# Kernel optimization log

Hardware: AMD Instinct MI355X
Metric: run time of the kernel (lower is better)

## Reference

```python
import jax, jax.numpy as jnp
import numpy as np

B, S, E = 8, 4096, 128

def _prelu(x, a):
    return jnp.where(x >= 0, x, a * x)

def setup_inputs() -> dict:
    key = jax.random.key(0)
    ks = jax.random.split(key, 7)
    lim = 1.0 / np.sqrt(E)
    x = jax.random.normal(ks[0], (B, S, E), dtype=jnp.float32)
    Wq = jax.random.uniform(ks[1], (E, E), jnp.float32, -lim, lim)
    Wk = jax.random.uniform(ks[2], (E, E), jnp.float32, -lim, lim)
    Wv = jax.random.uniform(ks[3], (E, E), jnp.float32, -lim, lim)
    bq = jax.random.uniform(ks[4], (E,), jnp.float32, -lim, lim)
    bk = jax.random.uniform(ks[5], (E,), jnp.float32, -lim, lim)
    bv = jax.random.uniform(ks[6], (E,), jnp.float32, -lim, lim)
    # PReLU default: single shared slope initialized to 0.25
    aq = jnp.array(0.25, dtype=jnp.float32)
    ak = jnp.array(0.25, dtype=jnp.float32)
    av = jnp.array(0.25, dtype=jnp.float32)
    return {"x": x, "Wq": Wq, "bq": bq, "aq": aq,
            "Wk": Wk, "bk": bk, "ak": ak,
            "Wv": Wv, "bv": bv, "av": av}

def reference(x, Wq, bq, aq, Wk, bk, ak, Wv, bv, av):
    # Linear (y = x @ W.T + b) followed by PReLU, per nn.Sequential(Linear, PReLU)
    qx = _prelu(jnp.einsum('bse,fe->bsf', x, Wq) + bq, aq)  # [B,S,E]
    kx = _prelu(jnp.einsum('bse,fe->bsf', x, Wk) + bk, ak)
    vx = _prelu(jnp.einsum('bse,fe->bsf', x, Wv) + bv, av)
    scale = 1.0 / jnp.sqrt(jnp.asarray(E, dtype=x.dtype))
    qk = jnp.einsum('bqe,bke->bqk', qx, kx) * scale  # [B,S,S]
    attn = jax.nn.softmax(qk, axis=2)
    return jnp.einsum('bqk,bke->bqe', attn, vx)  # [B,S,E]
```

## Files before the change

kernel.cpp:

```cpp
#include <hip/hip_runtime.h>
#include <hip/hip_bf16.h>
#include <stdint.h>

typedef __bf16 bf16x8 __attribute__((ext_vector_type(8)));
typedef float f32x4 __attribute__((ext_vector_type(4)));
typedef float f32x16 __attribute__((ext_vector_type(16)));
typedef unsigned int u32x4 __attribute__((ext_vector_type(4)));

static constexpr int Bn = 8, Sn = 4096, En = 128;

__device__ __forceinline__ unsigned short f2bf(float f) {
  unsigned u = __builtin_bit_cast(unsigned, f);
  u += 0x7fffu + ((u >> 16) & 1u);
  return (unsigned short)(u >> 16);
}

__device__ __forceinline__ unsigned cvtpk(float a, float b) {
  unsigned r;
  asm("v_cvt_pk_bf16_f32 %0, %1, %2" : "=v"(r) : "v"(a), "v"(b));
  return r;
}

__device__ __forceinline__ void plswap(unsigned &a, unsigned &b) {
  asm("v_permlane32_swap_b32 %0, %1" : "+v"(a), "+v"(b));
}

__global__ __launch_bounds__(256) void qkv_kernel(
    const float* __restrict__ x,
    const float* __restrict__ Wq, const float* __restrict__ bq, const float* __restrict__ aq,
    const float* __restrict__ Wk, const float* __restrict__ bk, const float* __restrict__ ak,
    const float* __restrict__ Wv, const float* __restrict__ bv, const float* __restrict__ av,
    unsigned short* __restrict__ qo, unsigned short* __restrict__ kf,
    unsigned short* __restrict__ vf)
{
  __shared__ __align__(16) unsigned short xs[64 * 136];
  __shared__ __align__(16) unsigned short wsh[128 * 136];
  const int tid = threadIdx.x;
  const int r0 = blockIdx.x * 64;

  for (int i = 0; i < 8; ++i) {
    int cid = tid + i * 256;
    int row = cid >> 5, c4 = cid & 31;
    const float4 v = *(const float4*)&x[(size_t)(r0 + row) * 128 + c4 * 4];
    unsigned short* d = &xs[row * 136 + c4 * 4];
    d[0] = f2bf(v.x); d[1] = f2bf(v.y); d[2] = f2bf(v.z); d[3] = f2bf(v.w);
  }

  const int lane = tid & 63, wid = tid >> 6;
  const int g = lane >> 4, ln = lane & 15;
  const float* Ws[3] = {Wq, Wk, Wv};
  const float* Bs[3] = {bq, bk, bv};
  const float* As[3] = {aq, ak, av};
  bf16x8 afrag[4];

  for (int mat = 0; mat < 3; ++mat) {
    __syncthreads();
    for (int i = 0; i < 16; ++i) {
      int cid = tid + i * 256;
      int row = cid >> 5, c4 = cid & 31;
      const float4 v = *(const float4*)&Ws[mat][row * 128 + c4 * 4];
      unsigned short* d = &wsh[row * 136 + c4 * 4];
      d[0] = f2bf(v.x); d[1] = f2bf(v.y); d[2] = f2bf(v.z); d[3] = f2bf(v.w);
    }
    __syncthreads();

    if (mat == 0) {
      for (int ks = 0; ks < 4; ++ks)
        afrag[ks] = *(const bf16x8*)&xs[(wid * 16 + ln) * 136 + ks * 32 + g * 8];
    }
    const float alpha = As[mat][0];
    f32x4 acc[8];
    for (int nt = 0; nt < 8; ++nt) acc[nt] = (f32x4)(0.f);
    for (int nt = 0; nt < 8; ++nt)
      for (int ks = 0; ks < 4; ++ks) {
        bf16x8 bfrag = *(const bf16x8*)&wsh[(nt * 16 + ln) * 136 + ks * 32 + g * 8];
        acc[nt] = __builtin_amdgcn_mfma_f32_16x16x32_bf16(afrag[ks], bfrag, acc[nt], 0, 0, 0);
      }
    const int mbase = r0 + wid * 16 + g * 4;
    for (int nt = 0; nt < 8; ++nt) {
      const int n = nt * 16 + ln;
      const float bias = Bs[mat][n];
      float vv[4];
      for (int r = 0; r < 4; ++r) {
        float t = acc[nt][r] + bias;
        vv[r] = t >= 0.f ? t : alpha * t;
      }
      if (mat == 0) {
        for (int r = 0; r < 4; ++r) qo[(size_t)(mbase + r) * 128 + n] = f2bf(vv[r]);
      } else if (mat == 1) {
        for (int r = 0; r < 4; ++r) {
          const int key = mbase + r, bb = key >> 12, sl = key & 4095;
          const size_t addr = ((size_t)bb << 20) + (size_t)(sl >> 5) * 8192
                            + nt * 1024 + ((ln >> 3) & 1) * 512
                            + (sl & 31) * 16 + ((ln & 7) << 1);
          *(unsigned short*)((char*)kf + addr) = f2bf(vv[r]);
        }
      } else {
        const int bb = mbase >> 12, sl = mbase & 4095;
        const int kb64 = sl >> 6, kk = sl & 63;
        const int ks2 = kk >> 4, hi2 = (kk >> 3) & 1, j0 = kk & 7;
        const size_t addr = ((size_t)bb << 20) + (size_t)kb64 * 16384
                          + (n >> 5) * 4096 + ks2 * 1024 + hi2 * 512
                          + (n & 31) * 16 + (j0 << 1);
        ushort4 pk;
        pk.x = f2bf(vv[0]); pk.y = f2bf(vv[1]); pk.z = f2bf(vv[2]); pk.w = f2bf(vv[3]);
        *(ushort4*)((char*)vf + addr) = pk;
      }
    }
  }
}

__device__ __forceinline__ void load_frag(const char* kfb, const char* vfb, int kt,
                                          int tid, uint4* kr, uint4* vr) {
  const char* ks = kfb + (size_t)kt * 16384;
  const char* vs = vfb + (size_t)kt * 16384;
  kr[0] = *(const uint4*)(ks + tid * 16);
  kr[1] = *(const uint4*)(ks + 8192 + tid * 16);
  vr[0] = *(const uint4*)(vs + tid * 16);
  vr[1] = *(const uint4*)(vs + 8192 + tid * 16);
}

__device__ __forceinline__ void store_frag(char* slot, int tid,
                                           const uint4* kr, const uint4* vr) {
  *(uint4*)(slot + tid * 16) = kr[0];
  *(uint4*)(slot + 8192 + tid * 16) = kr[1];
  *(uint4*)(slot + 16384 + tid * 16) = vr[0];
  *(uint4*)(slot + 24576 + tid * 16) = vr[1];
}

template <int KSPLIT>
__global__ __launch_bounds__(512, 2) void attn_kernel(
    const unsigned short* __restrict__ q,
    const unsigned short* __restrict__ kf,
    const unsigned short* __restrict__ vf,
    float* __restrict__ opart, float* __restrict__ mpart,
    float* __restrict__ lpart, float* __restrict__ out)
{
  __shared__ __align__(16) char smem[98304];
  const int tid = threadIdx.x;
  const int lane = tid & 63, wid = tid >> 6;
  const int NS = 8 * KSPLIT;
  const int bid = blockIdx.x;
  const int s_ = bid % NS;
  const int qt = bid / NS;
  const int b  = s_ / KSPLIT;
  const int kh = s_ % KSPLIT;
  const int hi = lane >> 5, ln = lane & 31;
  const size_t bOff = (size_t)b * Sn * En;

  const int nkt = (Sn / KSPLIT) / 64;
  const int kbase = kh * (Sn / KSPLIT);
  const char* kfb = (const char*)kf + ((size_t)b << 20) + (size_t)(kbase >> 5) * 8192;
  const char* vfb = (const char*)vf + ((size_t)b << 20) + (size_t)(kbase >> 6) * 16384;

  const int qrow = qt * 256 + wid * 32 + ln;
  bf16x8 qf[8];
  #pragma unroll
  for (int s = 0; s < 8; ++s)
    qf[s] = *(const bf16x8*)((const char*)(q + bOff) + (size_t)qrow * 256 + s * 32 + hi * 16);

  f32x16 acc[4];
  #pragma unroll
  for (int et = 0; et < 4; ++et) acc[et] = (f32x16)(0.f);
  float m_run = -1e30f, lsum = 0.f;

  const float cst = 1.4426950408889634f * 0.08838834764831845f;

  auto qk = [&](const char* slot, f32x16& st0, f32x16& st1) {
    const char* kp = slot + hi * 512 + ln * 16;
    st0 = (f32x16)(0.f); st1 = (f32x16)(0.f);
    __builtin_amdgcn_s_setprio(1);
    #pragma unroll
    for (int s = 0; s < 8; ++s) {
      bf16x8 kf0 = *(const bf16x8*)(kp + s * 1024);
      bf16x8 kf1 = *(const bf16x8*)(kp + 8192 + s * 1024);
      st0 = __builtin_amdgcn_mfma_f32_32x32x16_bf16(kf0, qf[s], st0, 0, 0, 0);
      st1 = __builtin_amdgcn_mfma_f32_32x32x16_bf16(kf1, qf[s], st1, 0, 0, 0);
    }
    __builtin_amdgcn_s_setprio(0);
  };

  auto sm_pv = [&](const char* slot, const f32x16& st0, const f32x16& st1) {
    const char* vp = slot + 16384 + hi * 512 + ln * 16;
    float t16[16];
    #pragma unroll
    for (int i = 0; i < 16; ++i) t16[i] = fmaxf(st0[i], st1[i]);
    float t8[8];
    #pragma unroll
    for (int i = 0; i < 8; ++i) t8[i] = fmaxf(t16[i], t16[i + 8]);
    float t4[4];
    #pragma unroll
    for (int i = 0; i < 4; ++i) t4[i] = fmaxf(t8[i], t8[i + 4]);
    float vtile = fmaxf(fmaxf(t4[0], t4[1]), fmaxf(t4[2], t4[3])) * cst;
    vtile = fmaxf(vtile, __shfl_xor(vtile, 32));

    if (__any(vtile > m_run + 8.0f)) {
      float mnew = fmaxf(m_run, vtile);
      float al = __builtin_amdgcn_exp2f(m_run - mnew);
      #pragma unroll
      for (int et = 0; et < 4; ++et) acc[et] *= al;
      lsum *= al;
      m_run = mnew;
    }

    float p[32];
    #pragma unroll
    for (int i = 0; i < 16; ++i) p[i]      = __builtin_amdgcn_exp2f(fmaf(st0[i], cst, -m_run));
    #pragma unroll
    for (int i = 0; i < 16; ++i) p[16 + i] = __builtin_amdgcn_exp2f(fmaf(st1[i], cst, -m_run));

    float s16[16];
    #pragma unroll
    for (int i = 0; i < 16; ++i) s16[i] = p[i] + p[16 + i];
    float s8[8];
    #pragma unroll
    for (int i = 0; i < 8; ++i) s8[i] = s16[i] + s16[i + 8];
    float s4[4];
    #pragma unroll
    for (int i = 0; i < 4; ++i) s4[i] = s8[i] + s8[i + 4];
    float tsum = (s4[0] + s4[1]) + (s4[2] + s4[3]);
    tsum += __shfl_xor(tsum, 32);
    lsum += tsum;

    unsigned wa[8], wb[8];
    #pragma unroll
    for (int g2 = 0; g2 < 8; ++g2) {
      wa[g2] = cvtpk(p[4 * g2], p[4 * g2 + 1]);
      wb[g2] = cvtpk(p[4 * g2 + 2], p[4 * g2 + 3]);
    }
    bf16x8 pb[4];
    #pragma unroll
    for (int ks = 0; ks < 4; ++ks) {
      unsigned w0 = wa[2 * ks], w2 = wa[2 * ks + 1];
      plswap(w0, w2);
      unsigned w1 = wb[2 * ks], w3 = wb[2 * ks + 1];
      plswap(w1, w3);
      u32x4 w = {w0, w1, w2, w3};
      pb[ks] = __builtin_bit_cast(bf16x8, w);
    }

    __builtin_amdgcn_s_setprio(1);
    #pragma unroll
    for (int ks = 0; ks < 4; ++ks) {
      #pragma unroll
      for (int et = 0; et < 4; ++et) {
        bf16x8 vfr = *(const bf16x8*)(vp + et * 4096 + ks * 1024);
        acc[et] = __builtin_amdgcn_mfma_f32_32x32x16_bf16(vfr, pb[ks], acc[et], 0, 0, 0);
      }
    }
    __builtin_amdgcn_s_setprio(0);
  };

  char* s0 = smem;
  char* s1 = smem + 32768;
  char* s2 = smem + 65536;

  uint4 kregA[2], vregA[2], kregB[2], vregB[2];
  load_frag(kfb, vfb, 0, tid, kregA, vregA);
  store_frag(s0, tid, kregA, vregA);
  load_frag(kfb, vfb, 1, tid, kregB, vregB);
  store_frag(s1, tid, kregB, vregB);
  if (nkt > 2) load_frag(kfb, vfb, 2, tid, kregA, vregA);
  __syncthreads();
  f32x16 sA0, sA1, sB0, sB1;
  qk(s0, sA0, sA1);

  for (int t = 0; t < nkt; t += 2) {
    if (t + 2 < nkt) store_frag(s2, tid, kregA, vregA);
    if (t + 3 < nkt) load_frag(kfb, vfb, t + 3, tid, kregB, vregB);
    qk(s1, sB0, sB1);
    sm_pv(s0, sA0, sA1);
    __syncthreads();

    if (t + 3 < nkt) store_frag(s0, tid, kregB, vregB);
    if (t + 4 < nkt) load_frag(kfb, vfb, t + 4, tid, kregA, vregA);
    if (t + 2 < nkt) qk(s2, sA0, sA1);
    sm_pv(s1, sB0, sB1);
    __syncthreads();

    char* tt = s0; s0 = s2; s2 = s1; s1 = tt;
  }

  if (KSPLIT > 1 && lane < 32) {
    const size_t idx = (size_t)kh * (Bn * Sn) + (size_t)b * Sn + qt * 256 + wid * 32 + ln;
    mpart[idx] = m_run;
    lpart[idx] = lsum;
  }

  __syncthreads();
  const float inv = (KSPLIT == 1) ? (1.0f / lsum) : 1.0f;
  char* sl = smem + wid * 8192;
  char* outb;
  if (KSPLIT == 1)
    outb = (char*)(out + ((size_t)b * Sn + qt * 256 + wid * 32) * En);
  else
    outb = (char*)(opart + ((size_t)kh * (Bn * Sn) + (size_t)b * Sn + qt * 256 + wid * 32) * En);

  #pragma unroll
  for (int h = 0; h < 2; ++h) {
    #pragma unroll
    for (int e2 = 0; e2 < 2; ++e2) {
      const int et = 2 * h + e2;
      #pragma unroll
      for (int rg = 0; rg < 4; ++rg) {
        f32x4 v;
        #pragma unroll
        for (int j = 0; j < 4; ++j) v[j] = acc[et][rg * 4 + j] * inv;
        const int addr = ln * 256 + e2 * 128 + rg * 32 + hi * 16;
        *(f32x4*)(sl + (addr ^ ((ln & 7) << 4))) = v;
      }
    }
    asm volatile("s_waitcnt lgkmcnt(0)" ::: "memory");
    __builtin_amdgcn_sched_barrier(0);
    #pragma unroll
    for (int i = 0; i < 8; ++i) {
      const int flat = i * 1024 + lane * 16;
      const int qr = flat >> 8, col = flat & 255;
      f32x4 v = *(const f32x4*)(sl + ((qr * 256 + col) ^ ((qr & 7) << 4)));
      *(f32x4*)(outb + (size_t)qr * 512 + h * 256 + col) = v;
    }
    if (h == 0) {
      asm volatile("s_waitcnt lgkmcnt(0)" ::: "memory");
      __builtin_amdgcn_sched_barrier(0);
    }
  }
}

template <int NSPLIT>
__global__ __launch_bounds__(256) void combine_kernel(
    const float* __restrict__ op, const float* __restrict__ mp,
    const float* __restrict__ lp, float* __restrict__ out)
{
  const int idx = blockIdx.x * 256 + threadIdx.x;
  const int row = idx >> 5;
  const int BS = Bn * Sn;
  const size_t NO = (size_t)BS * En / 4;
  float m = -1e30f;
  #pragma unroll
  for (int j = 0; j < NSPLIT; ++j) m = fmaxf(m, mp[j * BS + row]);
  float den = 0.f;
  f32x4 sum = (f32x4)(0.f);
  #pragma unroll
  for (int j = 0; j < NSPLIT; ++j) {
    const float w = __builtin_amdgcn_exp2f(mp[j * BS + row] - m);
    den += w * lp[j * BS + row];
    f32x4 o = ((const f32x4*)op)[j * NO + idx];
    sum += o * w;
  }
  const float inv = 1.f / den;
  ((f32x4*)out)[idx] = sum * inv;
}

extern "C" void kernel_launch(void* const* d_in, const int* in_sizes, int n_in,
                              void* d_out, int out_size, void* d_ws, size_t ws_size,
                              hipStream_t stream) {
  const float* x  = (const float*)d_in[0];
  const float* Wq = (const float*)d_in[1];
  const float* bq = (const float*)d_in[2];
  const float* aq = (const float*)d_in[3];
  const float* Wk = (const float*)d_in[4];
  const float* bk = (const float*)d_in[5];
  const float* ak = (const float*)d_in[6];
  const float* Wv = (const float*)d_in[7];
  const float* bv = (const float*)d_in[8];
  const float* av = (const float*)d_in[9];

  const size_t BSE = (size_t)Bn * Sn * En;
  const size_t BS  = (size_t)Bn * Sn;
  char* base = (char*)d_ws;
  unsigned short* qws = (unsigned short*)base;
  unsigned short* kws = qws + BSE;
  unsigned short* vws = kws + BSE;
  const size_t fixed = 3 * BSE * 2;
  float* opart = (float*)(base + fixed);

  auto need = [&](int j) { return fixed + (size_t)j * BSE * 4 + (size_t)j * BS * 8; };
  int split = 1;
  if (ws_size >= need(2)) split = 2;

  float* mpart = (float*)(base + fixed + (size_t)split * BSE * 4);
  float* lpart = mpart + (size_t)split * BS;

  qkv_kernel<<<512, 256, 0, stream>>>(x, Wq, bq, aq, Wk, bk, ak, Wv, bv, av,
                                      qws, kws, vws);
  if (split == 2) {
    attn_kernel<2><<<256, 512, 0, stream>>>(qws, kws, vws, opart, mpart, lpart,
                                            (float*)d_out);
    combine_kernel<2><<<4096, 256, 0, stream>>>(opart, mpart, lpart, (float*)d_out);
  } else {
    attn_kernel<1><<<128, 512, 0, stream>>>(qws, kws, vws, opart, mpart, lpart,
                                            (float*)d_out);
  }
}
```

Before: 142.8 us.

## Load K fragments directly from global into registers, staging only V in LDS

K tiles are no longer staged through shared memory. Each wave now loads its own K fragments straight from global memory into a 16-register prefetch buffer, one tile ahead of the QK MFMAs, and only V goes through the triple-buffered LDS ring. This cuts LDS traffic and shrinks shared memory from 96KB to 64KB. In exchange, every wave reads the same K tile from global/L2 separately (8x redundancy per block) and register pressure rises under the 512x2 launch bounds.

```diff
diff --git a/kernel.cpp b/kernel.cpp
--- a/kernel.cpp
+++ b/kernel.cpp
@@ -110,22 +110,15 @@
   }
 }
 
-__device__ __forceinline__ void load_frag(const char* kfb, const char* vfb, int kt,
-                                          int tid, uint4* kr, uint4* vr) {
-  const char* ks = kfb + (size_t)kt * 16384;
+__device__ __forceinline__ void load_vfrag(const char* vfb, int kt, int tid, uint4* vr) {
   const char* vs = vfb + (size_t)kt * 16384;
-  kr[0] = *(const uint4*)(ks + tid * 16);
-  kr[1] = *(const uint4*)(ks + 8192 + tid * 16);
   vr[0] = *(const uint4*)(vs + tid * 16);
   vr[1] = *(const uint4*)(vs + 8192 + tid * 16);
 }
 
-__device__ __forceinline__ void store_frag(char* slot, int tid,
-                                           const uint4* kr, const uint4* vr) {
-  *(uint4*)(slot + tid * 16) = kr[0];
-  *(uint4*)(slot + 8192 + tid * 16) = kr[1];
-  *(uint4*)(slot + 16384 + tid * 16) = vr[0];
-  *(uint4*)(slot + 24576 + tid * 16) = vr[1];
+__device__ __forceinline__ void store_vfrag(char* slot, int tid, const uint4* vr) {
+  *(uint4*)(slot + tid * 16) = vr[0];
+  *(uint4*)(slot + 8192 + tid * 16) = vr[1];
 }
 
 template <int KSPLIT>
@@ -136,7 +129,7 @@
     float* __restrict__ opart, float* __restrict__ mpart,
     float* __restrict__ lpart, float* __restrict__ out)
 {
-  __shared__ __align__(16) char smem[98304];
+  __shared__ __align__(16) char smem[65536];
   const int tid = threadIdx.x;
   const int lane = tid & 63, wid = tid >> 6;
   const int NS = 8 * KSPLIT;
@@ -166,22 +159,29 @@
 
   const float cst = 1.4426950408889634f * 0.08838834764831845f;
 
-  auto qk = [&](const char* slot, f32x16& st0, f32x16& st1) {
-    const char* kp = slot + hi * 512 + ln * 16;
+  bf16x8 kfr[16];
+  auto load_k = [&](int kt) {
+    const char* kp = kfb + (size_t)kt * 16384 + hi * 512 + ln * 16;
+    #pragma unroll
+    for (int s = 0; s < 8; ++s) {
+      kfr[s]     = *(const bf16x8*)(kp + s * 1024);
+      kfr[8 + s] = *(const bf16x8*)(kp + 8192 + s * 1024);
+    }
+  };
+
+  auto qk = [&](f32x16& st0, f32x16& st1) {
     st0 = (f32x16)(0.f); st1 = (f32x16)(0.f);
     __builtin_amdgcn_s_setprio(1);
     #pragma unroll
     for (int s = 0; s < 8; ++s) {
-      bf16x8 kf0 = *(const bf16x8*)(kp + s * 1024);
-      bf16x8 kf1 = *(const bf16x8*)(kp + 8192 + s * 1024);
-      st0 = __builtin_amdgcn_mfma_f32_32x32x16_bf16(kf0, qf[s], st0, 0, 0, 0);
-      st1 = __builtin_amdgcn_mfma_f32_32x32x16_bf16(kf1, qf[s], st1, 0, 0, 0);
+      st0 = __builtin_amdgcn_mfma_f32_32x32x16_bf16(kfr[s], qf[s], st0, 0, 0, 0);
+      st1 = __builtin_amdgcn_mfma_f32_32x32x16_bf16(kfr[8 + s], qf[s], st1, 0, 0, 0);
     }
     __builtin_amdgcn_s_setprio(0);
   };
 
   auto sm_pv = [&](const char* slot, const f32x16& st0, const f32x16& st1) {
-    const char* vp = slot + 16384 + hi * 512 + ln * 16;
+    const char* vp = slot + hi * 512 + ln * 16;
     float t16[16];
     #pragma unroll
     for (int i = 0; i < 16; ++i) t16[i] = fmaxf(st0[i], st1[i]);
@@ -252,29 +252,33 @@
   };
 
   char* s0 = smem;
-  char* s1 = smem + 32768;
-  char* s2 = smem + 65536;
-
-  uint4 kregA[2], vregA[2], kregB[2], vregB[2];
-  load_frag(kfb, vfb, 0, tid, kregA, vregA);
-  store_frag(s0, tid, kregA, vregA);
-  load_frag(kfb, vfb, 1, tid, kregB, vregB);
-  store_frag(s1, tid, kregB, vregB);
-  if (nkt > 2) load_frag(kfb, vfb, 2, tid, kregA, vregA);
+  char* s1 = smem + 16384;
+  char* s2 = smem + 32768;
+
+  uint4 vregA[2], vregB[2];
+  load_vfrag(vfb, 0, tid, vregA);
+  store_vfrag(s0, tid, vregA);
+  load_vfrag(vfb, 1, tid, vregB);
+  store_vfrag(s1, tid, vregB);
+  if (nkt > 2) load_vfrag(vfb, 2, tid, vregA);
+  load_k(0);
   __syncthreads();
   f32x16 sA0, sA1, sB0, sB1;
-  qk(s0, sA0, sA1);
+  qk(sA0, sA1);
+  load_k(1);
 
   for (int t = 0; t < nkt; t += 2) {
-    if (t + 2 < nkt) store_frag(s2, tid, kregA, vregA);
-    if (t + 3 < nkt) load_frag(kfb, vfb, t + 3, tid, kregB, vregB);
-    qk(s1, sB0, sB1);
+    if (t + 2 < nkt) store_vfrag(s2, tid, vregA);
+    if (t + 3 < nkt) load_vfrag(vfb, t + 3, tid, vregB);
+    qk(sB0, sB1);
+    if (t + 2 < nkt) load_k(t + 2);
     sm_pv(s0, sA0, sA1);
     __syncthreads();
 
-    if (t + 3 < nkt) store_frag(s0, tid, kregB, vregB);
-    if (t + 4 < nkt) load_frag(kfb, vfb, t + 4, tid, kregA, vregA);
-    if (t + 2 < nkt) qk(s2, sA0, sA1);
+    if (t + 3 < nkt) store_vfrag(s0, tid, vregB);
+    if (t + 4 < nkt) load_vfrag(vfb, t + 4, tid, vregA);
+    if (t + 2 < nkt) qk(sA0, sA1);
+    if (t + 3 < nkt) load_k(t + 3);
     sm_pv(s1, sB0, sB1);
     __syncthreads();
 
```

After: 219.6 us. 53.8% more time.
